# Performance work log

Measured on AMD Instinct MI355X. Metric: run time of the kernel, lower is better.

Reference implementation:

```python
import jax, jax.numpy as jnp
import numpy as np

B, C, H, S, DC = 32768, 1024, 1024, 8, 64  # batch, num_classes, hidden_dim, num_styles, calibrator dim

def setup_inputs() -> dict:
    key = jax.random.key(0)
    ks = jax.random.split(key, 12)
    inp = {
        "logits": jax.random.normal(ks[0], (B, C), dtype=jnp.float32),
        "style_idx": jax.random.randint(ks[1], (B,), 0, S, dtype=jnp.int32),
        # learned params
        "style_emb": jax.random.normal(ks[2], (S, H), dtype=jnp.float32),
        "Wa1": jax.random.normal(ks[3], (C + H, H), dtype=jnp.float32) * (1.0 / np.sqrt(C + H)),
        "ba1": jnp.zeros((H,), dtype=jnp.float32),
        "Wa2": jax.random.normal(ks[4], (H, C), dtype=jnp.float32) * (1.0 / np.sqrt(H)),
        "ba2": jnp.zeros((C,), dtype=jnp.float32),
        # per-style confidence calibrators: Linear(C,64) -> ReLU -> Linear(64,1) -> Sigmoid
        "Wc1": jax.random.normal(ks[5], (S, C, DC), dtype=jnp.float32) * (1.0 / np.sqrt(C)),
        "bc1": jnp.zeros((S, DC), dtype=jnp.float32),
        "Wc2": jax.random.normal(ks[6], (S, DC), dtype=jnp.float32) * (1.0 / np.sqrt(DC)),
        "bc2": jnp.zeros((S,), dtype=jnp.float32),
    }
    return inp

def reference(logits, style_idx, style_emb, Wa1, ba1, Wa2, ba2, Wc1, bc1, Wc2, bc2):
    # style embedding lookup + adapter MLP (residual on logits)
    emb = style_emb[style_idx]                                  # (B, H)
    combined = jnp.concatenate([logits, emb], axis=1)           # (B, C+H)
    hidden = jax.nn.relu(combined @ Wa1 + ba1)                  # (B, H)
    adjusted_logits = logits + hidden @ Wa2 + ba2               # (B, C)
    probs = jax.nn.softmax(adjusted_logits, axis=1)             # (B, C)
    # expert-routed confidence calibration: compute all styles densely, select per sample
    h = jax.nn.relu(jnp.einsum('bc,scd->bsd', probs, Wc1) + bc1)   # (B, S, DC)
    conf_all = jax.nn.sigmoid(jnp.einsum('bsd,sd->bs', h, Wc2) + bc2)  # (B, S)
    calibrated_confidence = jnp.take_along_axis(conf_all, style_idx[:, None].astype(jnp.int32), axis=1)  # (B, 1)
    return adjusted_logits, calibrated_confidence
```

## Files before the change

### kernel.cpp

```cpp
#include <hip/hip_runtime.h>
#include <hip/hip_bf16.h>
#include <stdint.h>

typedef __hip_bfloat16 bf16;
typedef __attribute__((ext_vector_type(8))) short short8;
typedef __attribute__((ext_vector_type(4))) float f32x4;

#define NB 32768
#define NC 1024
#define NH 1024
#define NS 8
#define NDC 64

__device__ __forceinline__ void gload_lds16(const void* g, void* l) {
    __builtin_amdgcn_global_load_lds((const __attribute__((address_space(1))) void*)g,
                                     (__attribute__((address_space(3))) void*)l, 16, 0, 0);
}

__device__ __forceinline__ short f2bf(float x) {
    bf16 h = __float2bfloat16(x);
    short s;
    __builtin_memcpy(&s, &h, 2);
    return s;
}

__global__ __launch_bounds__(256) void convert_kernel(
    const float* __restrict__ in, bf16* __restrict__ out)
{
    const size_t i = ((size_t)blockIdx.x * 256 + threadIdx.x) * 8;
    float4 a = *(const float4*)(in + i);
    float4 b = *(const float4*)(in + i + 4);
    short8 v;
    v[0] = f2bf(a.x); v[1] = f2bf(a.y); v[2] = f2bf(a.z); v[3] = f2bf(a.w);
    v[4] = f2bf(b.x); v[5] = f2bf(b.y); v[6] = f2bf(b.z); v[7] = f2bf(b.w);
    *(short8*)((short*)out + i) = v;
}

__global__ __launch_bounds__(256) void transpose_kernel(
    const float* __restrict__ in, bf16* __restrict__ out,
    int R, int Ccols, long long in_bs, long long out_bs)
{
    __shared__ float tile[32][33];
    const float* inb = in + (long long)blockIdx.z * in_bs;
    bf16* outb = out + (long long)blockIdx.z * out_bs;
    int c0 = blockIdx.x * 32, r0 = blockIdx.y * 32;
    int tx = threadIdx.x, ty = threadIdx.y;
#pragma unroll
    for (int i = 0; i < 32; i += 8)
        tile[ty + i][tx] = inb[(size_t)(r0 + ty + i) * Ccols + c0 + tx];
    __syncthreads();
#pragma unroll
    for (int i = 0; i < 32; i += 8)
        outb[(size_t)(c0 + ty + i) * R + r0 + tx] = __float2bfloat16(tile[tx][ty + i]);
}

__global__ __launch_bounds__(256) void style_partial_kernel(
    const float* __restrict__ style_emb, const float* __restrict__ Wa1,
    float* __restrict__ partial)
{
    const int h = (blockIdx.x & 3) * 256 + threadIdx.x;
    const int ks = blockIdx.x >> 2;
    float acc[NS];
#pragma unroll
    for (int s = 0; s < NS; ++s) acc[s] = 0.f;
#pragma unroll
    for (int kk = 0; kk < 16; ++kk) {
        const int k = ks * 16 + kk;
        const float w = Wa1[(size_t)(NC + k) * NH + h];
#pragma unroll
        for (int s = 0; s < NS; ++s)
            acc[s] += style_emb[s * NH + k] * w;
    }
#pragma unroll
    for (int s = 0; s < NS; ++s)
        partial[((size_t)ks * NS + s) * NH + h] = acc[s];
}

__global__ __launch_bounds__(256) void style_reduce_kernel(
    const float* __restrict__ partial, const float* __restrict__ ba1,
    float* __restrict__ out)
{
    const int i = blockIdx.x * 256 + threadIdx.x;
    const int h = i & (NH - 1);
    const int s = i >> 10;
    float acc = ba1[h];
#pragma unroll 8
    for (int ks = 0; ks < 64; ++ks)
        acc += partial[((size_t)ks * NS + s) * NH + h];
    out[i] = acc;
}

template<int MODE>
__global__ __launch_bounds__(256, 2) void gemm_kernel(
    const bf16* __restrict__ A, const bf16* __restrict__ BT,
    bf16* __restrict__ Cb, float* __restrict__ Cf,
    int N, int K,
    const float* __restrict__ style_contrib, const int* __restrict__ style_idx,
    const float* __restrict__ resid, const float* __restrict__ bias,
    const float* __restrict__ bc1, const float* __restrict__ Wc2,
    const float* __restrict__ bc2, float* __restrict__ conf_out)
{
    __shared__ short lds[3 * 2 * 128 * 32];

    const int t = threadIdx.x;
    const int lane = t & 63;
    const int wave = t >> 6;
    const int wr = wave >> 1;
    const int wc = wave & 1;

    const int nwg = gridDim.x * gridDim.y;
    const int flat = blockIdx.y * gridDim.x + blockIdx.x;
    const int cpx = nwg >> 3;
    const int swz = (flat & 7) * cpx + (flat >> 3);
    const int bm0 = (swz / gridDim.x) * 128;
    const int bn0 = (swz % gridDim.x) * 128;

    const int tp = t ^ (((t >> 5) & 1) << 1);
    const int r0 = tp >> 2;
    const int c8 = (tp & 3) * 8;

    const int mrow = lane & 15;
    const int quad = lane >> 4;
    const int qx8 = (quad ^ (((lane >> 3) & 1) << 1)) * 8;

    f32x4 acc[4][4];
#pragma unroll
    for (int i = 0; i < 4; ++i)
#pragma unroll
        for (int j = 0; j < 4; ++j) acc[i][j] = (f32x4){0.f, 0.f, 0.f, 0.f};

    const bf16* gA = A + (size_t)(bm0 + r0) * K + c8;
    const bf16* gB = BT + (size_t)(bn0 + r0) * K + c8;

    const int K32 = K >> 5;

#define STAGE(kt, ob)                                                          \
    do {                                                                       \
        short* dst_ = lds + (ob);                                              \
        gload_lds16(gA + (kt) * 32, dst_ + t * 8);                             \
        gload_lds16(gA + (size_t)64 * K + (kt) * 32, dst_ + 2048 + t * 8);     \
        gload_lds16(gB + (kt) * 32, dst_ + 4096 + t * 8);                      \
        gload_lds16(gB + (size_t)64 * K + (kt) * 32, dst_ + 6144 + t * 8);     \
    } while (0)

    int ocur = 0, onxt = 8192, othr = 16384;
    STAGE(0, ocur);
    STAGE(1, onxt);

    for (int kt = 0; kt < K32; ++kt) {
        if (kt + 1 < K32)
            asm volatile("s_waitcnt vmcnt(4)\n\ts_barrier" ::: "memory");
        else
            asm volatile("s_waitcnt vmcnt(0)\n\ts_barrier" ::: "memory");

        if (kt + 2 < K32) STAGE(kt + 2, othr);

        const short* pA = lds + ocur;
        const short* pB = lds + ocur + 4096;
        short8 af[4], bfr[4];
#pragma unroll
        for (int i = 0; i < 4; ++i)
            af[i] = *(const short8*)(pA + (wr * 64 + i * 16 + mrow) * 32 + qx8);
#pragma unroll
        for (int j = 0; j < 4; ++j)
            bfr[j] = *(const short8*)(pB + (wc * 64 + j * 16 + mrow) * 32 + qx8);
#pragma unroll
        for (int i = 0; i < 4; ++i)
#pragma unroll
            for (int j = 0; j < 4; ++j)
                acc[i][j] = __builtin_amdgcn_mfma_f32_16x16x32_bf16(af[i], bfr[j], acc[i][j], 0, 0, 0);

        const int tmp = ocur; ocur = onxt; onxt = othr; othr = tmp;
    }
#undef STAGE

    if (MODE == 2) {
        const int s_w = (bn0 >> 6) + wc;
        float bcv[4], wcv[4];
#pragma unroll
        for (int j = 0; j < 4; ++j) {
            const int d = j * 16 + mrow;
            bcv[j] = bc1[s_w * NDC + d];
            wcv[j] = Wc2[s_w * NDC + d];
        }
        const float bias2 = bc2[s_w];
#pragma unroll
        for (int i = 0; i < 4; ++i) {
#pragma unroll
            for (int r = 0; r < 4; ++r) {
                const int grow = bm0 + wr * 64 + i * 16 + quad * 4 + r;
                float p = 0.f;
#pragma unroll
                for (int j = 0; j < 4; ++j)
                    p += fmaxf(acc[i][j][r] + bcv[j], 0.f) * wcv[j];
#pragma unroll
                for (int off = 1; off < 16; off <<= 1) p += __shfl_xor(p, off, 64);
                if (mrow == 0 && style_idx[grow] == s_w)
                    conf_out[grow] = 1.0f / (1.0f + __expf(-(p + bias2)));
            }
        }
        return;
    }

#pragma unroll
    for (int i = 0; i < 4; ++i) {
#pragma unroll
        for (int r = 0; r < 4; ++r) {
            const int grow = bm0 + wr * 64 + i * 16 + quad * 4 + r;
            const float* scrow = nullptr;
            const float* resrow = nullptr;
            if (MODE == 0) scrow = style_contrib + (size_t)style_idx[grow] * N;
            if (MODE == 1) resrow = resid + (size_t)grow * N;
#pragma unroll
            for (int j = 0; j < 4; ++j) {
                const int gcol = bn0 + wc * 64 + j * 16 + mrow;
                float v = acc[i][j][r];
                if (MODE == 0) {
                    v += scrow[gcol];
                    v = fmaxf(v, 0.f);
                    Cb[(size_t)grow * N + gcol] = __float2bfloat16(v);
                } else {
                    v += resrow[gcol] + bias[gcol];
                    Cf[(size_t)grow * N + gcol] = v;
                }
            }
        }
    }
}

__global__ __launch_bounds__(256) void softmax_kernel(
    const float* __restrict__ in, bf16* __restrict__ out)
{
    const size_t row = blockIdx.x;
    const float* x = in + row * NC;
    bf16* o = out + row * NC;
    const int t = threadIdx.x;
    __shared__ float red[8];

    float v[4];
    float m = -1e30f;
#pragma unroll
    for (int i = 0; i < 4; ++i) {
        v[i] = x[t + i * 256];
        m = fmaxf(m, v[i]);
    }
#pragma unroll
    for (int off = 1; off < 64; off <<= 1) m = fmaxf(m, __shfl_xor(m, off, 64));
    const int wv = t >> 6;
    if ((t & 63) == 0) red[wv] = m;
    __syncthreads();
    const float gm = fmaxf(fmaxf(red[0], red[1]), fmaxf(red[2], red[3]));

    float s = 0.f;
#pragma unroll
    for (int i = 0; i < 4; ++i) {
        v[i] = __expf(v[i] - gm);
        s += v[i];
    }
#pragma unroll
    for (int off = 1; off < 64; off <<= 1) s += __shfl_xor(s, off, 64);
    if ((t & 63) == 0) red[4 + wv] = s;
    __syncthreads();
    const float inv = 1.0f / (red[4] + red[5] + red[6] + red[7]);
#pragma unroll
    for (int i = 0; i < 4; ++i) o[t + i * 256] = __float2bfloat16(v[i] * inv);
}

extern "C" void kernel_launch(void* const* d_in, const int* in_sizes, int n_in,
                              void* d_out, int out_size, void* d_ws, size_t ws_size,
                              hipStream_t stream) {
    const float* logits    = (const float*)d_in[0];
    const int*   style_idx = (const int*)d_in[1];
    const float* style_emb = (const float*)d_in[2];
    const float* Wa1       = (const float*)d_in[3];
    const float* ba1       = (const float*)d_in[4];
    const float* Wa2       = (const float*)d_in[5];
    const float* ba2       = (const float*)d_in[6];
    const float* Wc1       = (const float*)d_in[7];
    const float* bc1       = (const float*)d_in[8];
    const float* Wc2       = (const float*)d_in[9];
    const float* bc2       = (const float*)d_in[10];

    char* ws = (char*)d_ws;
    bf16* logits_b = (bf16*)ws;        ws += (size_t)NB * NC * 2;
    bf16* hidden = (bf16*)ws;          ws += (size_t)NB * NH * 2;
    bf16* W1T = (bf16*)ws;             ws += (size_t)NC * NH * 2;
    bf16* W2T = (bf16*)ws;             ws += (size_t)NH * NC * 2;
    bf16* Wc1T = (bf16*)ws;            ws += (size_t)NS * NDC * NC * 2;
    float* style_contrib = (float*)ws; ws += (size_t)NS * NH * 4;
    float* style_partial = (float*)ws; ws += (size_t)64 * NS * NH * 4;

    float* adjusted = (float*)d_out;
    float* conf_out = (float*)d_out + (size_t)NB * NC;

    convert_kernel<<<(NB * NC) / (256 * 8), 256, 0, stream>>>(logits, logits_b);

    dim3 tb(32, 8);
    transpose_kernel<<<dim3(32, 32, 1), tb, 0, stream>>>(Wa1, W1T, NC, NH, 0, 0);
    transpose_kernel<<<dim3(32, 32, 1), tb, 0, stream>>>(Wa2, W2T, NH, NC, 0, 0);
    transpose_kernel<<<dim3(2, 32, NS), tb, 0, stream>>>(Wc1, Wc1T, NC, NDC,
                                                         (long long)NC * NDC, (long long)NDC * NC);
    style_partial_kernel<<<256, 256, 0, stream>>>(style_emb, Wa1, style_partial);
    style_reduce_kernel<<<NS * NH / 256, 256, 0, stream>>>(style_partial, ba1, style_contrib);

    gemm_kernel<0><<<dim3(NH / 128, NB / 128), 256, 0, stream>>>(
        logits_b, W1T, hidden, nullptr, NH, NC, style_contrib, style_idx, nullptr, nullptr,
        nullptr, nullptr, nullptr, nullptr);
    gemm_kernel<1><<<dim3(NC / 128, NB / 128), 256, 0, stream>>>(
        hidden, W2T, nullptr, adjusted, NC, NH, nullptr, nullptr, logits, ba2,
        nullptr, nullptr, nullptr, nullptr);
    softmax_kernel<<<NB, 256, 0, stream>>>(adjusted, hidden);
    gemm_kernel<2><<<dim3((NS * NDC) / 128, NB / 128), 256, 0, stream>>>(
        hidden, Wc1T, nullptr, nullptr, NS * NDC, NC, nullptr, style_idx, nullptr, nullptr,
        bc1, Wc2, bc2, conf_out);
}
```

Before: 540.5 us.

## Fuse fp32-to-bf16 logits conversion into first GEMM and switch to BK=64 single-buffered tiles

Removes the standalone convert kernel and its bf16 logits buffer; the first GEMM now loads fp32 logits directly, converts to bf16 in registers and writes them into swizzled LDS. All GEMMs move from a triple-buffered BK=32 async pipeline to a single-buffered BK=64 loop with XOR-swizzled LDS and two barriers per step. This saves the round trip through memory for the converted logits, but the fp32 A tile of the first GEMM is reread by every N-tile, and the loss of prefetch overlap may expose load latency in all three GEMMs.

After: 498.8 us. -7.7%, faster.

```diff
diff --git a/kernel.cpp b/kernel.cpp
--- a/kernel.cpp
+++ b/kernel.cpp
@@ -22,18 +22,6 @@
     short s;
     __builtin_memcpy(&s, &h, 2);
     return s;
-}
-
-__global__ __launch_bounds__(256) void convert_kernel(
-    const float* __restrict__ in, bf16* __restrict__ out)
-{
-    const size_t i = ((size_t)blockIdx.x * 256 + threadIdx.x) * 8;
-    float4 a = *(const float4*)(in + i);
-    float4 b = *(const float4*)(in + i + 4);
-    short8 v;
-    v[0] = f2bf(a.x); v[1] = f2bf(a.y); v[2] = f2bf(a.z); v[3] = f2bf(a.w);
-    v[4] = f2bf(b.x); v[5] = f2bf(b.y); v[6] = f2bf(b.z); v[7] = f2bf(b.w);
-    *(short8*)((short*)out + i) = v;
 }
 
 __global__ __launch_bounds__(256) void transpose_kernel(
@@ -92,7 +80,7 @@
 
 template<int MODE>
 __global__ __launch_bounds__(256, 2) void gemm_kernel(
-    const bf16* __restrict__ A, const bf16* __restrict__ BT,
+    const void* __restrict__ Ain, const bf16* __restrict__ BT,
     bf16* __restrict__ Cb, float* __restrict__ Cf,
     int N, int K,
     const float* __restrict__ style_contrib, const int* __restrict__ style_idx,
@@ -100,7 +88,8 @@
     const float* __restrict__ bc1, const float* __restrict__ Wc2,
     const float* __restrict__ bc2, float* __restrict__ conf_out)
 {
-    __shared__ short lds[3 * 2 * 128 * 32];
+    __shared__ short lA[128 * 64];
+    __shared__ short lB[128 * 64];
 
     const int t = threadIdx.x;
     const int lane = t & 63;
@@ -115,13 +104,13 @@
     const int bm0 = (swz / gridDim.x) * 128;
     const int bn0 = (swz % gridDim.x) * 128;
 
-    const int tp = t ^ (((t >> 5) & 1) << 1);
-    const int r0 = tp >> 2;
-    const int c8 = (tp & 3) * 8;
+    const int r08 = t >> 3;
+    const int clog = t & 7;
+    const int csrc = clog ^ (r08 & 7);
 
     const int mrow = lane & 15;
     const int quad = lane >> 4;
-    const int qx8 = (quad ^ (((lane >> 3) & 1) << 1)) * 8;
+    const int mrow7 = mrow & 7;
 
     f32x4 acc[4][4];
 #pragma unroll
@@ -129,50 +118,53 @@
 #pragma unroll
         for (int j = 0; j < 4; ++j) acc[i][j] = (f32x4){0.f, 0.f, 0.f, 0.f};
 
-    const bf16* gA = A + (size_t)(bm0 + r0) * K + c8;
-    const bf16* gB = BT + (size_t)(bn0 + r0) * K + c8;
-
-    const int K32 = K >> 5;
-
-#define STAGE(kt, ob)                                                          \
-    do {                                                                       \
-        short* dst_ = lds + (ob);                                              \
-        gload_lds16(gA + (kt) * 32, dst_ + t * 8);                             \
-        gload_lds16(gA + (size_t)64 * K + (kt) * 32, dst_ + 2048 + t * 8);     \
-        gload_lds16(gB + (kt) * 32, dst_ + 4096 + t * 8);                      \
-        gload_lds16(gB + (size_t)64 * K + (kt) * 32, dst_ + 6144 + t * 8);     \
-    } while (0)
-
-    int ocur = 0, onxt = 8192, othr = 16384;
-    STAGE(0, ocur);
-    STAGE(1, onxt);
-
-    for (int kt = 0; kt < K32; ++kt) {
-        if (kt + 1 < K32)
-            asm volatile("s_waitcnt vmcnt(4)\n\ts_barrier" ::: "memory");
-        else
-            asm volatile("s_waitcnt vmcnt(0)\n\ts_barrier" ::: "memory");
-
-        if (kt + 2 < K32) STAGE(kt + 2, othr);
-
-        const short* pA = lds + ocur;
-        const short* pB = lds + ocur + 4096;
-        short8 af[4], bfr[4];
-#pragma unroll
-        for (int i = 0; i < 4; ++i)
-            af[i] = *(const short8*)(pA + (wr * 64 + i * 16 + mrow) * 32 + qx8);
-#pragma unroll
-        for (int j = 0; j < 4; ++j)
-            bfr[j] = *(const short8*)(pB + (wc * 64 + j * 16 + mrow) * 32 + qx8);
-#pragma unroll
-        for (int i = 0; i < 4; ++i)
+    const float* gAf = (const float*)Ain + (size_t)(bm0 + r08) * K + clog * 8;
+    const bf16*  gAb = (const bf16*)Ain + (size_t)(bm0 + r08) * K + csrc * 8;
+    const bf16*  gB  = BT + (size_t)(bn0 + r08) * K + csrc * 8;
+
+    for (int k0 = 0; k0 < K; k0 += 64) {
+        if (MODE == 0) {
+#pragma unroll
+            for (int q = 0; q < 4; ++q) {
+                const int row = q * 32 + r08;
+                const float* src = gAf + (size_t)q * 32 * K + k0;
+                float4 a = *(const float4*)(src);
+                float4 b = *(const float4*)(src + 4);
+                short8 v;
+                v[0] = f2bf(a.x); v[1] = f2bf(a.y); v[2] = f2bf(a.z); v[3] = f2bf(a.w);
+                v[4] = f2bf(b.x); v[5] = f2bf(b.y); v[6] = f2bf(b.z); v[7] = f2bf(b.w);
+                *(short8*)(lA + row * 64 + (clog ^ (row & 7)) * 8) = v;
+            }
+        } else {
+#pragma unroll
+            for (int q = 0; q < 4; ++q)
+                gload_lds16(gAb + (size_t)q * 32 * K + k0, lA + q * 2048 + t * 8);
+        }
+#pragma unroll
+        for (int q = 0; q < 4; ++q)
+            gload_lds16(gB + (size_t)q * 32 * K + k0, lB + q * 2048 + t * 8);
+
+        __syncthreads();
+
+#pragma unroll
+        for (int kk = 0; kk < 2; ++kk) {
+            const int coff = ((kk * 4 + quad) ^ mrow7) * 8;
+            short8 af[4], bfr[4];
+#pragma unroll
+            for (int i = 0; i < 4; ++i)
+                af[i] = *(const short8*)(lA + (wr * 64 + i * 16 + mrow) * 64 + coff);
 #pragma unroll
             for (int j = 0; j < 4; ++j)
-                acc[i][j] = __builtin_amdgcn_mfma_f32_16x16x32_bf16(af[i], bfr[j], acc[i][j], 0, 0, 0);
-
-        const int tmp = ocur; ocur = onxt; onxt = othr; othr = tmp;
-    }
-#undef STAGE
+                bfr[j] = *(const short8*)(lB + (wc * 64 + j * 16 + mrow) * 64 + coff);
+#pragma unroll
+            for (int i = 0; i < 4; ++i)
+#pragma unroll
+                for (int j = 0; j < 4; ++j)
+                    acc[i][j] = __builtin_amdgcn_mfma_f32_16x16x32_bf16(af[i], bfr[j], acc[i][j], 0, 0, 0);
+        }
+
+        __syncthreads();
+    }
 
     if (MODE == 2) {
         const int s_w = (bn0 >> 6) + wc;
@@ -282,7 +274,6 @@
     const float* bc2       = (const float*)d_in[10];
 
     char* ws = (char*)d_ws;
-    bf16* logits_b = (bf16*)ws;        ws += (size_t)NB * NC * 2;
     bf16* hidden = (bf16*)ws;          ws += (size_t)NB * NH * 2;
     bf16* W1T = (bf16*)ws;             ws += (size_t)NC * NH * 2;
     bf16* W2T = (bf16*)ws;             ws += (size_t)NH * NC * 2;
@@ -292,8 +283,6 @@
 
     float* adjusted = (float*)d_out;
     float* conf_out = (float*)d_out + (size_t)NB * NC;
-
-    convert_kernel<<<(NB * NC) / (256 * 8), 256, 0, stream>>>(logits, logits_b);
 
     dim3 tb(32, 8);
     transpose_kernel<<<dim3(32, 32, 1), tb, 0, stream>>>(Wa1, W1T, NC, NH, 0, 0);
@@ -304,7 +293,7 @@
     style_reduce_kernel<<<NS * NH / 256, 256, 0, stream>>>(style_partial, ba1, style_contrib);
 
     gemm_kernel<0><<<dim3(NH / 128, NB / 128), 256, 0, stream>>>(
-        logits_b, W1T, hidden, nullptr, NH, NC, style_contrib, style_idx, nullptr, nullptr,
+        logits, W1T, hidden, nullptr, NH, NC, style_contrib, style_idx, nullptr, nullptr,
         nullptr, nullptr, nullptr, nullptr);
     gemm_kernel<1><<<dim3(NC / 128, NB / 128), 256, 0, stream>>>(
         hidden, W2T, nullptr, adjusted, NC, NH, nullptr, nullptr, logits, ba2,
```
